# Kernel optimization log

Measured on AMD Instinct MI355X. Metric: run time of the kernel, lower is better.

Reference implementation:

```python
import jax, jax.numpy as jnp
import numpy as np

N = 524288          # total atoms (sorted by degree)
E = 1433600         # total directed bonds
B, L = 16384, 32    # molecules x atoms-per-molecule (B*L == N)
NODE, EDGE, H, OUT = 64, 16, 128, 128
N0 = 8192           # number of degree-0 atoms
DEG_COUNTS = {1: 65536, 2: 131072, 3: 196608, 4: 98304, 5: 24576}
BN_EPS = 1e-5


def setup_inputs() -> dict:
    key = jax.random.key(0)
    ks = jax.random.split(key, 24)
    inp = {}
    inp["node_feat"] = jax.random.normal(ks[0], (N, NODE), jnp.float32)
    inp["edge_feat"] = jax.random.normal(ks[1], (E, EDGE), jnp.float32)
    i = 2
    for d in (1, 2, 3, 4, 5):
        n_d = DEG_COUNTS[d]
        inp[f"nbr_node_d{d}"] = jax.random.randint(ks[i], (n_d, d), 0, N, jnp.int32); i += 1
        inp[f"nbr_edge_d{d}"] = jax.random.randint(ks[i], (n_d, d), 0, E, jnp.int32); i += 1
    inp["atom_index"] = jnp.arange(B * L, dtype=jnp.int32).reshape(B, L)

    def lin(k, o, fan_in):
        return jax.random.normal(k, (o, fan_in), jnp.float32) / np.sqrt(fan_in).astype(np.float32)

    inp["out_W0"] = lin(ks[12], OUT, NODE); inp["out_b0"] = jnp.zeros((OUT,), jnp.float32)
    inp["out_W1"] = lin(ks[13], OUT, H);    inp["out_b1"] = jnp.zeros((OUT,), jnp.float32)
    inp["out_W2"] = lin(ks[14], OUT, H);    inp["out_b2"] = jnp.zeros((OUT,), jnp.float32)
    inp["conv0_selfW"] = lin(ks[15], H, NODE)
    inp["conv0_degW"] = jax.random.normal(ks[16], (5, H, NODE + EDGE), jnp.float32) / np.sqrt(NODE + EDGE).astype(np.float32)
    inp["conv0_bias"] = jnp.zeros((1, H), jnp.float32)
    inp["conv1_selfW"] = lin(ks[17], H, H)
    inp["conv1_degW"] = jax.random.normal(ks[18], (5, H, H + EDGE), jnp.float32) / np.sqrt(H + EDGE).astype(np.float32)
    inp["conv1_bias"] = jnp.zeros((1, H), jnp.float32)
    return inp


def _graph_degree_conv(node_repr, edge_repr, selfW, degW, bias, nbr_nodes, nbr_edges):
    out_size = selfW.shape[0]
    # degree 0: zero neighbor contribution
    parts = [jnp.zeros((N0, out_size), node_repr.dtype)]
    for di, d in enumerate((1, 2, 3, 4, 5)):
        nn_rep = node_repr[nbr_nodes[di]]          # [n_d, d, node]
        ee_rep = edge_repr[nbr_edges[di]]          # [n_d, d, edge]
        summed = jnp.concatenate([nn_rep.sum(1), ee_rep.sum(1)], axis=-1)  # [n_d, node+edge]
        parts.append(summed @ degW[di].T)          # per-degree linear (no bias)
    neighbor_repr = jnp.concatenate(parts, axis=0)  # nodes sorted by degree -> aligned
    act = node_repr @ selfW.T + neighbor_repr + bias
    # BatchNorm1d(affine=False), training-mode batch stats (biased variance)
    mean = act.mean(0)
    var = act.var(0)
    act = (act - mean) / jnp.sqrt(var + BN_EPS)
    return jax.nn.relu(act)


def reference(node_feat, edge_feat,
              nbr_node_d1, nbr_edge_d1, nbr_node_d2, nbr_edge_d2,
              nbr_node_d3, nbr_edge_d3, nbr_node_d4, nbr_edge_d4,
              nbr_node_d5, nbr_edge_d5, atom_index,
              out_W0, out_b0, out_W1, out_b1, out_W2, out_b2,
              conv0_selfW, conv0_degW, conv0_bias,
              conv1_selfW, conv1_degW, conv1_bias):
    nbr_nodes = (nbr_node_d1, nbr_node_d2, nbr_node_d3, nbr_node_d4, nbr_node_d5)
    nbr_edges = (nbr_edge_d1, nbr_edge_d2, nbr_edge_d3, nbr_edge_d4, nbr_edge_d5)

    x = node_feat
    acc = jax.nn.softmax(x @ out_W0.T + out_b0, axis=1)
    x = _graph_degree_conv(x, edge_feat, conv0_selfW, conv0_degW, conv0_bias, nbr_nodes, nbr_edges)
    acc = acc + jax.nn.softmax(x @ out_W1.T + out_b1, axis=1)
    x = _graph_degree_conv(x, edge_feat, conv1_selfW, conv1_degW, conv1_bias, nbr_nodes, nbr_edges)
    acc = acc + jax.nn.softmax(x @ out_W2.T + out_b2, axis=1)
    # scatter per-atom activations into [batch, max_len, OUT]
    return acc[atom_index]
```

## Files before the change

### kernel.cpp

```cpp
#include <hip/hip_runtime.h>
#include <math.h>


typedef short  short8   __attribute__((ext_vector_type(8)));
typedef unsigned short ushort8v __attribute__((ext_vector_type(8)));
typedef float  f32x4    __attribute__((ext_vector_type(4)));
typedef unsigned int u32;

static constexpr int  N_ATOMS = 524288;
static constexpr long NROWCOL = (long)N_ATOMS * 128;
static constexpr int  NBLK    = N_ATOMS / 64;

__device__ __forceinline__ ushort f2bf(float x) {
    unsigned u = __float_as_uint(x);
    return (ushort)((u + 0x7fffu + ((u >> 16) & 1u)) >> 16);
}
__device__ __forceinline__ float bf2f(ushort h) {
    return __uint_as_float(((unsigned)h) << 16);
}

__device__ __forceinline__ void gload_lds16(const ushort* g, ushort* l) {
    __builtin_amdgcn_global_load_lds(
        (const __attribute__((address_space(1))) u32*)g,
        (__attribute__((address_space(3))) u32*)l, 16, 0, 0);
}

__device__ __forceinline__ void seg_of(long r, int& d, long& off) {
    if      (r < 73728)  { d = 1; off = 8192;  }
    else if (r < 204800) { d = 2; off = 73728; }
    else if (r < 401408) { d = 3; off = 204800;}
    else if (r < 499712) { d = 4; off = 401408;}
    else                 { d = 5; off = 499712;}
}

__device__ __forceinline__ uint4 pack8(const float v[8]) {
    uint4 w;
    w.x = f2bf(v[0]) | ((unsigned)f2bf(v[1]) << 16);
    w.y = f2bf(v[2]) | ((unsigned)f2bf(v[3]) << 16);
    w.z = f2bf(v[4]) | ((unsigned)f2bf(v[5]) << 16);
    w.w = f2bf(v[6]) | ((unsigned)f2bf(v[7]) << 16);
    return w;
}
__device__ __forceinline__ short8 pack8s(const float v[8]) {
    short8 o;
#pragma unroll
    for (int e = 0; e < 8; ++e) o[e] = (short)f2bf(v[e]);
    return o;
}

__global__ __launch_bounds__(256)
void esum_kernel(const float* __restrict__ edge_feat,
                 const int* __restrict__ ne1, const int* __restrict__ ne2,
                 const int* __restrict__ ne3, const int* __restrict__ ne4,
                 const int* __restrict__ ne5, ushort* __restrict__ esumb)
{
    const long t = (long)blockIdx.x * 256 + threadIdx.x;
    const long r = 8192 + (t >> 1);
    const int  h = (int)(t & 1);
    int d; long off; seg_of(r, d, off);
    const int* ne = (d==1)?ne1:(d==2)?ne2:(d==3)?ne3:(d==4)?ne4:ne5;
    const long i0 = (r - off) * d;
    float v[8] = {0,0,0,0,0,0,0,0};
    for (int j = 0; j < d; ++j) {
        const long e = ne[i0 + j];
        const float4* p = (const float4*)(edge_feat + e * 16 + h * 8);
        const float4 a = p[0], b = p[1];
        v[0]+=a.x; v[1]+=a.y; v[2]+=a.z; v[3]+=a.w;
        v[4]+=b.x; v[5]+=b.y; v[6]+=b.z; v[7]+=b.w;
    }
    *(uint4*)(esumb + (r - 8192) * 16 + h * 8) = pack8(v);
}

__global__ void wprep(const float* __restrict__ src, ushort* __restrict__ dst,
                      int rows, int Ks, int Kd)
{
    const int i = blockIdx.x * 256 + threadIdx.x;
    if (i >= rows * Kd) return;
    const int r = i / Kd, c = i % Kd;
    dst[i] = f2bf(c < Ks ? src[r * Ks + c] : 0.f);
}

__global__ void wprep_img(const float* __restrict__ src, ushort* __restrict__ dst, int K)
{
    const int i = blockIdx.x * 256 + threadIdx.x;
    if (i >= 128 * K) return;
    const int row = i / K, col = i % K;
    dst[(col >> 3) * 1024 + row * 8 + (col & 7)] = f2bf(src[i]);
}

template<int NG, bool F32, bool BN>
__device__ __forceinline__ void stage_rows(const void* Xv, long r0,
                                           ushort* __restrict__ Ab,
                                           const float* __restrict__ statsL)
{
    for (int t = threadIdx.x; t < 64 * NG; t += 256) {
        const int row = t / NG, g = t % NG;
        const long gr = r0 + row;
        float v[8];
        if (F32) {
            const float4* p = (const float4*)((const float*)Xv + gr * (long)(NG * 8) + g * 8);
            const float4 a = p[0], b = p[1];
            v[0]=a.x; v[1]=a.y; v[2]=a.z; v[3]=a.w;
            v[4]=b.x; v[5]=b.y; v[6]=b.z; v[7]=b.w;
        } else {
            const ushort8v u = *(const ushort8v*)((const ushort*)Xv + gr * (long)(NG * 8) + g * 8);
#pragma unroll
            for (int e = 0; e < 8; ++e) v[e] = bf2f(u[e]);
        }
        if (BN) {
            const int c0 = g * 8;
#pragma unroll
            for (int e = 0; e < 8; ++e)
                v[e] = fmaxf(0.f, (v[e] - statsL[c0 + e]) * statsL[128 + c0 + e]);
        }
        ((uint4*)Ab)[row * NG + (g ^ (row & 7))] = pack8(v);
    }
}

template<int NGL, int NST, int NGN, bool F32, bool BN>
__device__ __forceinline__ void stage_gather(const void* Xv,
                                             const ushort* __restrict__ esumb,
                                             const int* __restrict__ nnl, int d,
                                             long r0, ushort* __restrict__ Ab,
                                             const float* __restrict__ statsL)
{
    for (int t = threadIdx.x; t < 64 * NST; t += 256) {
        const int row = t / NST, g = t % NST;
        float v[8] = {0,0,0,0,0,0,0,0};
        if (g < NGN) {
            const int c0 = g * 8;
            for (int j = 0; j < d; ++j) {
                const long idx = nnl[row * d + j];
                if (F32) {
                    const float4* p = (const float4*)((const float*)Xv + idx * (long)(NGN * 8) + c0);
                    const float4 a = p[0], b = p[1];
                    v[0]+=a.x; v[1]+=a.y; v[2]+=a.z; v[3]+=a.w;
                    v[4]+=b.x; v[5]+=b.y; v[6]+=b.z; v[7]+=b.w;
                } else {
                    const ushort8v u = *(const ushort8v*)((const ushort*)Xv + idx * (long)(NGN * 8) + c0);
#pragma unroll
                    for (int e = 0; e < 8; ++e) {
                        float x = bf2f(u[e]);
                        if (BN) x = fmaxf(0.f, (x - statsL[c0 + e]) * statsL[128 + c0 + e]);
                        v[e] += x;
                    }
                }
            }
        } else if (g < NGN + 2) {
            const long er = r0 + row - 8192;
            const ushort8v u = *(const ushort8v*)(esumb + er * 16 + (g - NGN) * 8);
#pragma unroll
            for (int e = 0; e < 8; ++e) v[e] = bf2f(u[e]);
        }
        ((uint4*)Ab)[row * NGL + (g ^ (row & 7))] = pack8(v);
    }
}

template<int KS, int NG>
__device__ __forceinline__ void mfma_lds(const ushort* __restrict__ Ab,
                                         const ushort* __restrict__ Wb, int KP,
                                         int wc, f32x4 acc[4][2])
{
    const int lane = threadIdx.x & 63;
    const int lg = lane >> 4, lr = lane & 15;
#pragma unroll
    for (int ks = 0; ks < KS; ++ks) {
        short8 B0 = *(const short8*)(Wb + (long)(wc + lr) * KP + ks * 32 + 8 * lg);
        short8 B1 = *(const short8*)(Wb + (long)(wc + 16 + lr) * KP + ks * 32 + 8 * lg);
        const int gk = ks * 4 + lg;
#pragma unroll
        for (int m = 0; m < 4; ++m) {
            const int row = 16 * m + lr;
            const short8 a = *(const short8*)(Ab + (row * NG + (gk ^ (row & 7))) * 8);
            acc[m][0] = __builtin_amdgcn_mfma_f32_16x16x32_bf16(a, B0, acc[m][0], 0, 0, 0);
            acc[m][1] = __builtin_amdgcn_mfma_f32_16x16x32_bf16(a, B1, acc[m][1], 0, 0, 0);
        }
    }
}

template<int K1, bool A1F32, bool BNIN, int NGL2, int NST2, int NGN2, int KS2, int KP2>
__global__ __launch_bounds__(256, 2)
void conv_kernel(const void* __restrict__ X, const ushort* __restrict__ Wb1,
                 const ushort* __restrict__ Wb2base,
                 const int* __restrict__ nn1, const int* __restrict__ nn2,
                 const int* __restrict__ nn3, const int* __restrict__ nn4,
                 const int* __restrict__ nn5,
                 const ushort* __restrict__ esumb, const float* __restrict__ cbias,
                 const float* __restrict__ stats_in,
                 ushort* __restrict__ act_out, float* __restrict__ part)
{
    constexpr int NG1 = K1 / 8;
    constexpr int KS1 = K1 / 32;
    constexpr int NGMAX = (NGL2 > NG1) ? NGL2 : NG1;
    __shared__ uint4 AbV[64 * NGMAX];
    __shared__ int   nnl[320];
    __shared__ float statsL[256];
    ushort* Ab = (ushort*)AbV;

    const long r0 = (long)blockIdx.x * 64;
    const int wid = threadIdx.x >> 6, lane = threadIdx.x & 63;
    const int lg = lane >> 4, lr = lane & 15, wc = wid * 32;

    if (BNIN)
        for (int t = threadIdx.x; t < 256; t += 256) statsL[t] = stats_in[t];

    int d = 0;
    const bool has2 = (r0 >= 8192);
    if (has2) {
        long off; seg_of(r0, d, off);
        const int* nn = (d==1)?nn1:(d==2)?nn2:(d==3)?nn3:(d==4)?nn4:nn5;
        const long i0 = (r0 - off) * d;
        for (int t = threadIdx.x; t < 64 * d; t += 256) nnl[t] = nn[i0 + t];
    }
    __syncthreads();

    stage_rows<NG1, A1F32, BNIN>(X, r0, Ab, statsL);
    __syncthreads();
    f32x4 acc[4][2] = {};
    mfma_lds<KS1, NG1>(Ab, Wb1, K1, wc, acc);

    if (has2) {
        __syncthreads();
        stage_gather<NGL2, NST2, NGN2, A1F32, BNIN>(X, esumb, nnl, d, r0, Ab, statsL);
        __syncthreads();
        const ushort* Wb2 = Wb2base + (long)(d - 1) * 128 * KP2;
        mfma_lds<KS2, NGL2>(Ab, Wb2, KP2, wc, acc);
    }

#pragma unroll
    for (int n = 0; n < 2; ++n) {
        const float bv = cbias[wc + n * 16 + lr];
#pragma unroll
        for (int m = 0; m < 4; ++m)
#pragma unroll
            for (int j = 0; j < 4; ++j) acc[m][n][j] += bv;
    }
#pragma unroll
    for (int m = 0; m < 4; ++m)
#pragma unroll
        for (int j = 0; j < 4; ++j) {
            const long row = r0 + 16 * m + 4 * lg + j;
#pragma unroll
            for (int n = 0; n < 2; ++n)
                act_out[row * 128 + wc + n * 16 + lr] = f2bf(acc[m][n][j]);
        }
#pragma unroll
    for (int n = 0; n < 2; ++n) {
        float s = 0.f, q = 0.f;
#pragma unroll
        for (int m = 0; m < 4; ++m)
#pragma unroll
            for (int j = 0; j < 4; ++j) { const float v = acc[m][n][j]; s += v; q += v * v; }
        s += __shfl_xor(s, 16); s += __shfl_xor(s, 32);
        q += __shfl_xor(q, 16); q += __shfl_xor(q, 32);
        if (lane < 16) {
            part[(long)blockIdx.x * 256 + wc + n * 16 + lr]       = s;
            part[(long)blockIdx.x * 256 + 128 + wc + n * 16 + lr] = q;
        }
    }
}

__global__ __launch_bounds__(256)
void bn_finalize(const float* __restrict__ part, float* __restrict__ stats)
{
    const int c = blockIdx.x;
    float s = 0.f, q = 0.f;
    for (int b = threadIdx.x; b < NBLK; b += 256) {
        s += part[(long)b * 256 + c];
        q += part[(long)b * 256 + 128 + c];
    }
#pragma unroll
    for (int o = 1; o < 64; o <<= 1) { s += __shfl_xor(s, o); q += __shfl_xor(q, o); }
    __shared__ float rs[4], rq[4];
    const int wid = threadIdx.x >> 6;
    if ((threadIdx.x & 63) == 0) { rs[wid] = s; rq[wid] = q; }
    __syncthreads();
    if (threadIdx.x == 0) {
        s = rs[0] + rs[1] + rs[2] + rs[3];
        q = rq[0] + rq[1] + rq[2] + rq[3];
        const float mean = s * (1.0f / N_ATOMS);
        const float var  = q * (1.0f / N_ATOMS) - mean * mean;
        stats[c]       = mean;
        stats[128 + c] = 1.0f / sqrtf(var + 1e-5f);
    }
}

__device__ __forceinline__ void mfma8_img(const ushort* __restrict__ Wl, int base,
                                          int ks, int lg, int lr,
                                          short8 af, f32x4 (&acc)[8])
{
    const int a0 = base + (ks * 4 + lg) * 1024 + lr * 8;
#pragma unroll
    for (int n = 0; n < 8; ++n) {
        const short8 bf = *(const short8*)(Wl + a0 + n * 128);
        acc[n] = __builtin_amdgcn_mfma_f32_16x16x32_bf16(af, bf, acc[n], 0, 0, 0);
    }
}

__device__ __forceinline__ short8 cvt_bn(short8 u, int k0, const float* __restrict__ sl)
{
    float v[8];
#pragma unroll
    for (int e = 0; e < 8; ++e)
        v[e] = fmaxf(0.f, (bf2f((ushort)u[e]) - sl[k0 + e]) * sl[128 + k0 + e]);
    return pack8s(v);
}

__device__ __forceinline__ void softmax_accum(f32x4 (&acc)[8],
                                              const float* __restrict__ bias,
                                              int lr, f32x4 (&oacc)[8])
{
    float bb[8];
#pragma unroll
    for (int n = 0; n < 8; ++n) bb[n] = bias[n * 16 + lr];
#pragma unroll
    for (int j = 0; j < 4; ++j) {
        float mx = -1e30f;
#pragma unroll
        for (int n = 0; n < 8; ++n) { acc[n][j] += bb[n]; mx = fmaxf(mx, acc[n][j]); }
        mx = fmaxf(mx, __shfl_xor(mx, 1));
        mx = fmaxf(mx, __shfl_xor(mx, 2));
        mx = fmaxf(mx, __shfl_xor(mx, 4));
        mx = fmaxf(mx, __shfl_xor(mx, 8));
        float s = 0.f;
#pragma unroll
        for (int n = 0; n < 8; ++n) {
            const float e = __expf(acc[n][j] - mx);
            acc[n][j] = e; s += e;
        }
        s += __shfl_xor(s, 1); s += __shfl_xor(s, 2);
        s += __shfl_xor(s, 4); s += __shfl_xor(s, 8);
        const float inv = 1.0f / s;
#pragma unroll
        for (int n = 0; n < 8; ++n) oacc[n][j] += acc[n][j] * inv;
    }
}

__global__ __launch_bounds__(256, 2)
void out_kernel(const float* __restrict__ node, const ushort* __restrict__ act0b,
                const ushort* __restrict__ act1b, const ushort* __restrict__ wimg,
                const float* __restrict__ b0, const float* __restrict__ b1,
                const float* __restrict__ b2,
                const float* __restrict__ stats0, const float* __restrict__ stats1,
                float* __restrict__ out)
{
    __shared__ ushort Wlds[24576];
    __shared__ float sl[512];

    const int wid = threadIdx.x >> 6, lane = threadIdx.x & 63;
    const int lg = lane >> 4, lr = lane & 15;
    const long rA = (long)blockIdx.x * 64 + wid * 16 + lr;

#pragma unroll
    for (int i = 0; i < 12; ++i) {
        const int c = wid * 12 + i;
        gload_lds16(wimg + c * 512 + lane * 8, &Wlds[c * 512]);
    }
    for (int t = threadIdx.x; t < 512; t += 256)
        sl[t] = (t < 256) ? stats0[t] : stats1[t - 256];

    const float4* n0 = (const float4*)(node + rA * 64 + lg * 8);
    const float4* n1 = (const float4*)(node + rA * 64 + 32 + lg * 8);
    float4 h0a = n0[0], h0b = n0[1];
    float4 h1a = n1[0], h1b = n1[1];
    short8 r1[4];
#pragma unroll
    for (int ks = 0; ks < 4; ++ks)
        r1[ks] = *(const short8*)(act0b + rA * 128 + ks * 32 + lg * 8);

    __syncthreads();

    f32x4 oacc[8] = {};
    f32x4 acc[8] = {};
    {
        const float v0[8] = {h0a.x,h0a.y,h0a.z,h0a.w,h0b.x,h0b.y,h0b.z,h0b.w};
        mfma8_img(Wlds, 0, 0, lg, lr, pack8s(v0), acc);
        const float v1[8] = {h1a.x,h1a.y,h1a.z,h1a.w,h1b.x,h1b.y,h1b.z,h1b.w};
        mfma8_img(Wlds, 0, 1, lg, lr, pack8s(v1), acc);
    }
    short8 r2[4];
#pragma unroll
    for (int ks = 0; ks < 4; ++ks)
        r2[ks] = *(const short8*)(act1b + rA * 128 + ks * 32 + lg * 8);

    softmax_accum(acc, b0, lr, oacc);

    {
#pragma unroll
        for (int n = 0; n < 8; ++n) acc[n] = f32x4{0.f, 0.f, 0.f, 0.f};
#pragma unroll
        for (int ks = 0; ks < 4; ++ks) {
            const int k0 = ks * 32 + lg * 8;
            mfma8_img(Wlds, 8192, ks, lg, lr, cvt_bn(r1[ks], k0, sl), acc);
        }
        softmax_accum(acc, b1, lr, oacc);
    }

    __syncthreads();
#pragma unroll
    for (int i = 0; i < 8; ++i) {
        const int c = wid * 8 + i;
        gload_lds16(wimg + 24576 + c * 512 + lane * 8, &Wlds[8192 + c * 512]);
    }
    __syncthreads();

    {
#pragma unroll
        for (int n = 0; n < 8; ++n) acc[n] = f32x4{0.f, 0.f, 0.f, 0.f};
#pragma unroll
        for (int ks = 0; ks < 4; ++ks) {
            const int k0 = ks * 32 + lg * 8;
            mfma8_img(Wlds, 8192, ks, lg, lr, cvt_bn(r2[ks], k0, sl + 256), acc);
        }
        softmax_accum(acc, b2, lr, oacc);
    }

    const long rC0 = (long)blockIdx.x * 64 + wid * 16;
#pragma unroll
    for (int j = 0; j < 4; ++j) {
        const long row = rC0 + 4 * lg + j;
#pragma unroll
        for (int n = 0; n < 8; ++n)
            out[row * 128 + n * 16 + lr] = oacc[n][j];
    }
}

extern "C" void kernel_launch(void* const* d_in, const int* in_sizes, int n_in,
                              void* d_out, int out_size, void* d_ws, size_t ws_size,
                              hipStream_t stream)
{
    const float* node_feat = (const float*)d_in[0];
    const float* edge_feat = (const float*)d_in[1];
    const int* nn1 = (const int*)d_in[2];  const int* ne1 = (const int*)d_in[3];
    const int* nn2 = (const int*)d_in[4];  const int* ne2 = (const int*)d_in[5];
    const int* nn3 = (const int*)d_in[6];  const int* ne3 = (const int*)d_in[7];
    const int* nn4 = (const int*)d_in[8];  const int* ne4 = (const int*)d_in[9];
    const int* nn5 = (const int*)d_in[10]; const int* ne5 = (const int*)d_in[11];
    const float* W0     = (const float*)d_in[13];
    const float* b0     = (const float*)d_in[14];
    const float* W1     = (const float*)d_in[15];
    const float* b1     = (const float*)d_in[16];
    const float* W2     = (const float*)d_in[17];
    const float* b2     = (const float*)d_in[18];
    const float* selfW0 = (const float*)d_in[19];
    const float* degW0  = (const float*)d_in[20];
    const float* cb0    = (const float*)d_in[21];
    const float* selfW1 = (const float*)d_in[22];
    const float* degW1  = (const float*)d_in[23];
    const float* cb1    = (const float*)d_in[24];

    float*  part   = (float*)d_ws;
    float*  stats0 = part + (long)NBLK * 256;
    float*  stats1 = stats0 + 256;
    ushort* act0b  = (ushort*)(stats1 + 256);
    ushort* act1b  = act0b + NROWCOL;
    ushort* esumb  = act1b + NROWCOL;
    ushort* wb_self0 = esumb + (long)516096 * 16;
    ushort* wb_deg0  = wb_self0 + 128 * 64;
    ushort* wb_self1 = wb_deg0  + 640 * 96;
    ushort* wb_deg1  = wb_self1 + 128 * 128;
    ushort* wimg     = wb_deg1  + 640 * 160;
    const size_t needed = (size_t)((char*)(wimg + 40960) - (char*)d_ws);
    if (ws_size < needed) return;

    wprep<<<(128*64 +255)/256, 256, 0, stream>>>(selfW0, wb_self0, 128, 64, 64);
    wprep<<<(640*96 +255)/256, 256, 0, stream>>>(degW0,  wb_deg0,  640, 80, 96);
    wprep<<<(128*128+255)/256, 256, 0, stream>>>(selfW1, wb_self1, 128, 128, 128);
    wprep<<<(640*160+255)/256, 256, 0, stream>>>(degW1,  wb_deg1,  640, 144, 160);
    wprep_img<<<(128*64 +255)/256, 256, 0, stream>>>(W0, wimg,          64);
    wprep_img<<<(128*128+255)/256, 256, 0, stream>>>(W1, wimg + 8192,  128);
    wprep_img<<<(128*128+255)/256, 256, 0, stream>>>(W2, wimg + 24576, 128);

    esum_kernel<<<4032, 256, 0, stream>>>(edge_feat, ne1, ne2, ne3, ne4, ne5, esumb);

    conv_kernel<64, true, false, 16, 12, 8, 3, 96><<<NBLK, 256, 0, stream>>>(
        node_feat, wb_self0, wb_deg0, nn1, nn2, nn3, nn4, nn5, esumb, cb0, nullptr, act0b, part);
    bn_finalize<<<128, 256, 0, stream>>>(part, stats0);

    conv_kernel<128, false, true, 24, 20, 16, 5, 160><<<NBLK, 256, 0, stream>>>(
        act0b, wb_self1, wb_deg1, nn1, nn2, nn3, nn4, nn5, esumb, cb1, stats0, act1b, part);
    bn_finalize<<<128, 256, 0, stream>>>(part, stats1);

    out_kernel<<<NBLK, 256, 0, stream>>>(node_feat, act0b, act1b, wimg,
        b0, b1, b2, stats0, stats1, (float*)d_out);
}
```

Measured before the change: 572.0 us.

## Cut LDS in output kernel, fold BN into fma, skip bf16 repacking

Uses HIP's bf16 conversion intrinsics for packing. Copies bf16 data straight into LDS when no transform is needed. Precomputes BN as a scale and shift so normalization becomes one fma. Removes the max-subtraction from the softmax. Reorders out_kernel so it needs only a 16K-element weight LDS buffer, raising launch bounds to 4 blocks per CU. Dropping the softmax max risks overflow for large logits.

```diff
diff --git a/kernel.cpp b/kernel.cpp
--- a/kernel.cpp
+++ b/kernel.cpp
@@ -1,4 +1,5 @@
 #include <hip/hip_runtime.h>
+#include <hip/hip_bf16.h>
 #include <math.h>
 
 
@@ -11,12 +12,30 @@
 static constexpr long NROWCOL = (long)N_ATOMS * 128;
 static constexpr int  NBLK    = N_ATOMS / 64;
 
+__device__ __forceinline__ float bf2f(ushort h) {
+    return __uint_as_float(((unsigned)h) << 16);
+}
 __device__ __forceinline__ ushort f2bf(float x) {
     unsigned u = __float_as_uint(x);
     return (ushort)((u + 0x7fffu + ((u >> 16) & 1u)) >> 16);
 }
-__device__ __forceinline__ float bf2f(ushort h) {
-    return __uint_as_float(((unsigned)h) << 16);
+
+__device__ __forceinline__ uint4 pack8(const float v[8]) {
+    union { __hip_bfloat162 h2[4]; uint4 u; } c;
+#pragma unroll
+    for (int e = 0; e < 4; ++e)
+        c.h2[e] = __float22bfloat162_rn(make_float2(v[2*e], v[2*e+1]));
+    return c.u;
+}
+__device__ __forceinline__ short8 pack8s(const float v[8]) {
+    union { uint4 u; short8 s; } c;
+    c.u = pack8(v);
+    return c.s;
+}
+__device__ __forceinline__ ushort f2bf1(float x) {
+    union { __hip_bfloat16 b; ushort u; } c;
+    c.b = __float2bfloat16(x);
+    return c.u;
 }
 
 __device__ __forceinline__ void gload_lds16(const ushort* g, ushort* l) {
@@ -31,21 +50,6 @@
     else if (r < 401408) { d = 3; off = 204800;}
     else if (r < 499712) { d = 4; off = 401408;}
     else                 { d = 5; off = 499712;}
-}
-
-__device__ __forceinline__ uint4 pack8(const float v[8]) {
-    uint4 w;
-    w.x = f2bf(v[0]) | ((unsigned)f2bf(v[1]) << 16);
-    w.y = f2bf(v[2]) | ((unsigned)f2bf(v[3]) << 16);
-    w.z = f2bf(v[4]) | ((unsigned)f2bf(v[5]) << 16);
-    w.w = f2bf(v[6]) | ((unsigned)f2bf(v[7]) << 16);
-    return w;
-}
-__device__ __forceinline__ short8 pack8s(const float v[8]) {
-    short8 o;
-#pragma unroll
-    for (int e = 0; e < 8; ++e) o[e] = (short)f2bf(v[e]);
-    return o;
 }
 
 __global__ __launch_bounds__(256)
@@ -96,24 +100,24 @@
     for (int t = threadIdx.x; t < 64 * NG; t += 256) {
         const int row = t / NG, g = t % NG;
         const long gr = r0 + row;
-        float v[8];
+        uint4 w;
         if (F32) {
             const float4* p = (const float4*)((const float*)Xv + gr * (long)(NG * 8) + g * 8);
             const float4 a = p[0], b = p[1];
-            v[0]=a.x; v[1]=a.y; v[2]=a.z; v[3]=a.w;
-            v[4]=b.x; v[5]=b.y; v[6]=b.z; v[7]=b.w;
+            const float v[8] = {a.x,a.y,a.z,a.w,b.x,b.y,b.z,b.w};
+            w = pack8(v);
+        } else if (BN) {
+            const int c0 = g * 8;
+            const ushort8v u = *(const ushort8v*)((const ushort*)Xv + gr * (long)(NG * 8) + g * 8);
+            float v[8];
+#pragma unroll
+            for (int e = 0; e < 8; ++e)
+                v[e] = fmaxf(fmaf(bf2f(u[e]), statsL[c0 + e], statsL[128 + c0 + e]), 0.f);
+            w = pack8(v);
         } else {
-            const ushort8v u = *(const ushort8v*)((const ushort*)Xv + gr * (long)(NG * 8) + g * 8);
-#pragma unroll
-            for (int e = 0; e < 8; ++e) v[e] = bf2f(u[e]);
-        }
-        if (BN) {
-            const int c0 = g * 8;
-#pragma unroll
-            for (int e = 0; e < 8; ++e)
-                v[e] = fmaxf(0.f, (v[e] - statsL[c0 + e]) * statsL[128 + c0 + e]);
-        }
-        ((uint4*)Ab)[row * NG + (g ^ (row & 7))] = pack8(v);
+            w = *(const uint4*)((const ushort*)Xv + gr * (long)(NG * 8) + g * 8);
+        }
+        ((uint4*)Ab)[row * NG + (g ^ (row & 7))] = w;
     }
 }
 
@@ -126,9 +130,10 @@
 {
     for (int t = threadIdx.x; t < 64 * NST; t += 256) {
         const int row = t / NST, g = t % NST;
-        float v[8] = {0,0,0,0,0,0,0,0};
+        uint4 w = {0, 0, 0, 0};
         if (g < NGN) {
             const int c0 = g * 8;
+            float v[8] = {0,0,0,0,0,0,0,0};
             for (int j = 0; j < d; ++j) {
                 const long idx = nnl[row * d + j];
                 if (F32) {
@@ -141,18 +146,17 @@
 #pragma unroll
                     for (int e = 0; e < 8; ++e) {
                         float x = bf2f(u[e]);
-                        if (BN) x = fmaxf(0.f, (x - statsL[c0 + e]) * statsL[128 + c0 + e]);
+                        if (BN) x = fmaxf(fmaf(x, statsL[c0 + e], statsL[128 + c0 + e]), 0.f);
                         v[e] += x;
                     }
                 }
             }
+            w = pack8(v);
         } else if (g < NGN + 2) {
             const long er = r0 + row - 8192;
-            const ushort8v u = *(const ushort8v*)(esumb + er * 16 + (g - NGN) * 8);
-#pragma unroll
-            for (int e = 0; e < 8; ++e) v[e] = bf2f(u[e]);
-        }
-        ((uint4*)Ab)[row * NGL + (g ^ (row & 7))] = pack8(v);
+            w = *(const uint4*)(esumb + er * 16 + (g - NGN) * 8);
+        }
+        ((uint4*)Ab)[row * NGL + (g ^ (row & 7))] = w;
     }
 }
 
@@ -242,7 +246,7 @@
             const long row = r0 + 16 * m + 4 * lg + j;
 #pragma unroll
             for (int n = 0; n < 2; ++n)
-                act_out[row * 128 + wc + n * 16 + lr] = f2bf(acc[m][n][j]);
+                act_out[row * 128 + wc + n * 16 + lr] = f2bf1(acc[m][n][j]);
         }
 #pragma unroll
     for (int n = 0; n < 2; ++n) {
@@ -280,16 +284,17 @@
         q = rq[0] + rq[1] + rq[2] + rq[3];
         const float mean = s * (1.0f / N_ATOMS);
         const float var  = q * (1.0f / N_ATOMS) - mean * mean;
-        stats[c]       = mean;
-        stats[128 + c] = 1.0f / sqrtf(var + 1e-5f);
-    }
-}
-
-__device__ __forceinline__ void mfma8_img(const ushort* __restrict__ Wl, int base,
+        const float rstd = 1.0f / sqrtf(var + 1e-5f);
+        stats[c]       = rstd;
+        stats[128 + c] = -mean * rstd;
+    }
+}
+
+__device__ __forceinline__ void mfma8_img(const ushort* __restrict__ Wl,
                                           int ks, int lg, int lr,
                                           short8 af, f32x4 (&acc)[8])
 {
-    const int a0 = base + (ks * 4 + lg) * 1024 + lr * 8;
+    const int a0 = (ks * 4 + lg) * 1024 + lr * 8;
 #pragma unroll
     for (int n = 0; n < 8; ++n) {
         const short8 bf = *(const short8*)(Wl + a0 + n * 128);
@@ -302,7 +307,7 @@
     float v[8];
 #pragma unroll
     for (int e = 0; e < 8; ++e)
-        v[e] = fmaxf(0.f, (bf2f((ushort)u[e]) - sl[k0 + e]) * sl[128 + k0 + e]);
+        v[e] = fmaxf(fmaf(bf2f((ushort)u[e]), sl[k0 + e], sl[128 + k0 + e]), 0.f);
     return pack8s(v);
 }
 
@@ -315,17 +320,10 @@
     for (int n = 0; n < 8; ++n) bb[n] = bias[n * 16 + lr];
 #pragma unroll
     for (int j = 0; j < 4; ++j) {
-        float mx = -1e30f;
-#pragma unroll
-        for (int n = 0; n < 8; ++n) { acc[n][j] += bb[n]; mx = fmaxf(mx, acc[n][j]); }
-        mx = fmaxf(mx, __shfl_xor(mx, 1));
-        mx = fmaxf(mx, __shfl_xor(mx, 2));
-        mx = fmaxf(mx, __shfl_xor(mx, 4));
-        mx = fmaxf(mx, __shfl_xor(mx, 8));
         float s = 0.f;
 #pragma unroll
         for (int n = 0; n < 8; ++n) {
-            const float e = __expf(acc[n][j] - mx);
+            const float e = __expf(acc[n][j] + bb[n]);
             acc[n][j] = e; s += e;
         }
         s += __shfl_xor(s, 1); s += __shfl_xor(s, 2);
@@ -336,7 +334,7 @@
     }
 }
 
-__global__ __launch_bounds__(256, 2)
+__global__ __launch_bounds__(256, 4)
 void out_kernel(const float* __restrict__ node, const ushort* __restrict__ act0b,
                 const ushort* __restrict__ act1b, const ushort* __restrict__ wimg,
                 const float* __restrict__ b0, const float* __restrict__ b1,
@@ -344,7 +342,7 @@
                 const float* __restrict__ stats0, const float* __restrict__ stats1,
                 float* __restrict__ out)
 {
-    __shared__ ushort Wlds[24576];
+    __shared__ ushort Wlds[16384];
     __shared__ float sl[512];
 
     const int wid = threadIdx.x >> 6, lane = threadIdx.x & 63;
@@ -352,68 +350,72 @@
     const long rA = (long)blockIdx.x * 64 + wid * 16 + lr;
 
 #pragma unroll
-    for (int i = 0; i < 12; ++i) {
-        const int c = wid * 12 + i;
-        gload_lds16(wimg + c * 512 + lane * 8, &Wlds[c * 512]);
+    for (int i = 0; i < 8; ++i) {
+        const int c = wid * 8 + i;
+        gload_lds16(wimg + 8192 + c * 512 + lane * 8, &Wlds[c * 512]);
     }
     for (int t = threadIdx.x; t < 512; t += 256)
         sl[t] = (t < 256) ? stats0[t] : stats1[t - 256];
 
-    const float4* n0 = (const float4*)(node + rA * 64 + lg * 8);
-    const float4* n1 = (const float4*)(node + rA * 64 + 32 + lg * 8);
-    float4 h0a = n0[0], h0b = n0[1];
-    float4 h1a = n1[0], h1b = n1[1];
     short8 r1[4];
 #pragma unroll
     for (int ks = 0; ks < 4; ++ks)
         r1[ks] = *(const short8*)(act0b + rA * 128 + ks * 32 + lg * 8);
+    const float4* n0 = (const float4*)(node + rA * 64 + lg * 8);
+    float4 h0a = n0[0], h0b = n0[1];
 
     __syncthreads();
 
     f32x4 oacc[8] = {};
     f32x4 acc[8] = {};
     {
-        const float v0[8] = {h0a.x,h0a.y,h0a.z,h0a.w,h0b.x,h0b.y,h0b.z,h0b.w};
-        mfma8_img(Wlds, 0, 0, lg, lr, pack8s(v0), acc);
-        const float v1[8] = {h1a.x,h1a.y,h1a.z,h1a.w,h1b.x,h1b.y,h1b.z,h1b.w};
-        mfma8_img(Wlds, 0, 1, lg, lr, pack8s(v1), acc);
-    }
+#pragma unroll
+        for (int ks = 0; ks < 4; ++ks)
+            mfma8_img(Wlds, ks, lg, lr, cvt_bn(r1[ks], ks * 32 + lg * 8, sl), acc);
+    }
+    const float4* n1 = (const float4*)(node + rA * 64 + 32 + lg * 8);
+    float4 h1a = n1[0], h1b = n1[1];
     short8 r2[4];
 #pragma unroll
     for (int ks = 0; ks < 4; ++ks)
         r2[ks] = *(const short8*)(act1b + rA * 128 + ks * 32 + lg * 8);
 
+    softmax_accum(acc, b1, lr, oacc);
+
+    __syncthreads();
+#pragma unroll
+    for (int i = 0; i < 4; ++i) {
+        const int c = wid * 4 + i;
+        gload_lds16(wimg + c * 512 + lane * 8, &Wlds[c * 512]);
+    }
+    __syncthreads();
+
+#pragma unroll
+    for (int n = 0; n < 8; ++n) acc[n] = f32x4{0.f, 0.f, 0.f, 0.f};
+    {
+        const float v0[8] = {h0a.x,h0a.y,h0a.z,h0a.w,h0b.x,h0b.y,h0b.z,h0b.w};
+        mfma8_img(Wlds, 0, lg, lr, pack8s(v0), acc);
+        const float v1[8] = {h1a.x,h1a.y,h1a.z,h1a.w,h1b.x,h1b.y,h1b.z,h1b.w};
+        mfma8_img(Wlds, 1, lg, lr, pack8s(v1), acc);
+    }
     softmax_accum(acc, b0, lr, oacc);
-
-    {
-#pragma unroll
-        for (int n = 0; n < 8; ++n) acc[n] = f32x4{0.f, 0.f, 0.f, 0.f};
-#pragma unroll
-        for (int ks = 0; ks < 4; ++ks) {
-            const int k0 = ks * 32 + lg * 8;
-            mfma8_img(Wlds, 8192, ks, lg, lr, cvt_bn(r1[ks], k0, sl), acc);
-        }
-        softmax_accum(acc, b1, lr, oacc);
-    }
 
     __syncthreads();
 #pragma unroll
     for (int i = 0; i < 8; ++i) {
         const int c = wid * 8 + i;
-        gload_lds16(wimg + 24576 + c * 512 + lane * 8, &Wlds[8192 + c * 512]);
-    }
-    __syncthreads();
-
+        gload_lds16(wimg + 24576 + c * 512 + lane * 8, &Wlds[c * 512]);
+    }
+    __syncthreads();
+
+#pragma unroll
+    for (int n = 0; n < 8; ++n) acc[n] = f32x4{0.f, 0.f, 0.f, 0.f};
     {
 #pragma unroll
-        for (int n = 0; n < 8; ++n) acc[n] = f32x4{0.f, 0.f, 0.f, 0.f};
-#pragma unroll
-        for (int ks = 0; ks < 4; ++ks) {
-            const int k0 = ks * 32 + lg * 8;
-            mfma8_img(Wlds, 8192, ks, lg, lr, cvt_bn(r2[ks], k0, sl + 256), acc);
-        }
-        softmax_accum(acc, b2, lr, oacc);
-    }
+        for (int ks = 0; ks < 4; ++ks)
+            mfma8_img(Wlds, ks, lg, lr, cvt_bn(r2[ks], ks * 32 + lg * 8, sl + 256), acc);
+    }
+    softmax_accum(acc, b2, lr, oacc);
 
     const long rC0 = (long)blockIdx.x * 64 + wid * 16;
 #pragma unroll
@@ -474,11 +476,13 @@
     esum_kernel<<<4032, 256, 0, stream>>>(edge_feat, ne1, ne2, ne3, ne4, ne5, esumb);
 
     conv_kernel<64, true, false, 16, 12, 8, 3, 96><<<NBLK, 256, 0, stream>>>(
-        node_feat, wb_self0, wb_deg0, nn1, nn2, nn3, nn4, nn5, esumb, cb0, nullptr, act0b, part);
+        node_feat, wb_self0, wb_deg0, nn1, nn2, nn3, nn4, nn5, esumb, cb0,
+        nullptr, act0b, part);
     bn_finalize<<<128, 256, 0, stream>>>(part, stats0);
 
     conv_kernel<128, false, true, 24, 20, 16, 5, 160><<<NBLK, 256, 0, stream>>>(
-        act0b, wb_self1, wb_deg1, nn1, nn2, nn3, nn4, nn5, esumb, cb1, stats0, act1b, part);
+        act0b, wb_self1, wb_deg1, nn1, nn2, nn3, nn4, nn5, esumb, cb1,
+        stats0, act1b, part);
     bn_finalize<<<128, 256, 0, stream>>>(part, stats1);
 
     out_kernel<<<NBLK, 256, 0, stream>>>(node_feat, act0b, act1b, wimg,
```

Result: no change. 574.5 us (+0.4%).
